# Kernel tuning notes

Hardware: AMD Instinct MI355X
Metric: run time of the kernel (lower is better)

## Reference

```python
import jax, jax.numpy as jnp
import numpy as np

EPS = 1e-5


def setup_inputs() -> dict:
    key = jax.random.key(0)
    ks = jax.random.split(key, 10)
    B, C, H, W = 4, 256, 64, 64
    x = jax.random.normal(ks[0], (B, C, H, W), dtype=jnp.float32)
    s = 1.0 / np.sqrt(C)
    inp = {
        "x": x,
        "gn_w": jnp.ones((C,), jnp.float32),
        "gn_b": jnp.zeros((C,), jnp.float32),
        "wq": jax.random.normal(ks[1], (C, C), jnp.float32) * s,
        "bq": jnp.zeros((C,), jnp.float32),
        "wk": jax.random.normal(ks[2], (C, C), jnp.float32) * s,
        "bk": jnp.zeros((C,), jnp.float32),
        "wv": jax.random.normal(ks[3], (C, C), jnp.float32) * s,
        "bv": jnp.zeros((C,), jnp.float32),
        "wo": jax.random.normal(ks[4], (C, C), jnp.float32) * s,
        "bo": jnp.zeros((C,), jnp.float32),
    }
    return inp


def _forward(x, gn_w, gn_b, wq, bq, wk, bk, wv, bv, wo, bo):
    B, C, H, W = x.shape
    G = C // 2  # num_groups = channels // 2 -> 2 channels per group
    # GroupNorm
    xg = x.reshape(B, G, C // G, H, W)
    mu = jnp.mean(xg, axis=(2, 3, 4), keepdims=True)
    var = jnp.var(xg, axis=(2, 3, 4), keepdims=True)
    hn = ((xg - mu) * jax.lax.rsqrt(var + EPS)).reshape(B, C, H, W)
    hn = hn * gn_w[None, :, None, None] + gn_b[None, :, None, None]
    # tokens: (B, N, C), N = H*W
    h = hn.transpose(0, 2, 3, 1).reshape(B, H * W, C)
    q = h @ wq.T + bq
    k = h @ wk.T + bk
    v = h @ wv.T + bv
    # full NxN attention, scaled by C^-0.5 (as in original)
    scores = jnp.einsum("bnc,bmc->bnm", q, k) * (C ** -0.5)
    attn = jax.nn.softmax(scores, axis=-1)
    h2 = jnp.einsum("bnm,bmc->bnc", attn, v)  # (B, N, C)
    # faithful replication of the original's layout-scrambling reshape:
    # (B,N,C) -> (B,H,W,C) -> permute (B,C,H,W) -> reshape (B,HW,C)
    h2 = h2.reshape(B, H, W, C).transpose(0, 3, 1, 2).reshape(B, H * W, C)
    out = (h2 @ wo.T + bo).reshape(B, C, H, W)
    return x + out


def reference(x, gn_w, gn_b, wq, bq, wk, bk, wv, bv, wo, bo):
    return _forward(x, gn_w, gn_b, wq, bq, wk, bk, wv, bv, wo, bo)
```

## Files before the change

kernel.cpp:

```cpp
#include <hip/hip_runtime.h>

typedef unsigned short u16;
typedef unsigned int   u32;
typedef __attribute__((ext_vector_type(8)))  short short8;
typedef __attribute__((ext_vector_type(4)))  float f32x4;
typedef __attribute__((ext_vector_type(16))) float f32x16;

#define DI __device__ __forceinline__

DI u16 f2bf(float f){
  u32 u = __builtin_bit_cast(u32, f);
  u += 0x7fffu + ((u >> 16) & 1u);
  return (u16)(u >> 16);
}

DI void gl_lds16(const void* g, void* l){
  __builtin_amdgcn_global_load_lds((const __attribute__((address_space(1))) void*)g,
                                   (__attribute__((address_space(3))) void*)l, 16, 0, 0);
}

DI f32x4 mfma16(short8 a, short8 b, f32x4 c){
  return __builtin_amdgcn_mfma_f32_16x16x32_bf16(a, b, c, 0, 0, 0);
}
DI f32x16 mfma32(short8 a, short8 b, f32x16 c){
  return __builtin_amdgcn_mfma_f32_32x32x16_bf16(a, b, c, 0, 0, 0);
}
DI f32x16 z16(){
  f32x16 v;
  #pragma unroll
  for (int i=0;i<16;i++) v[i]=0.f;
  return v;
}

union U8 { u32 u[4]; short8 s; };

#define OFF_WBF   0u
#define OFF_STATS (512u<<10)
#define OFF_HTOK  (1u<<20)
#define OFF_Q     ((1u<<20) + (8u<<20))
#define OFF_K     ((1u<<20) + (16u<<20))
#define OFF_VT    ((1u<<20) + (24u<<20))
#define OFF_H2T   OFF_Q
#define OFF_PART  ((1u<<20) + (32u<<20))
#define OFF_ML    ((1u<<20) + (96u<<20))

__global__ void k_prepstats(const float* wq, const float* wk, const float* wv, const float* wo,
                            u16* wbf, const float* x, float2* stats){
  const int bid = blockIdx.x;
  if (bid < 256){
    const int wi = bid >> 6;
    const float* src = (wi==0)?wq:(wi==1)?wk:(wi==2)?wv:wo;
    u16* d = wbf + wi*65536;
    int i = ((bid&63)*256 + threadIdx.x)*4;
    float4 v = *(const float4*)(src + i);
    u32 lo = (u32)f2bf(v.x) | ((u32)f2bf(v.y)<<16);
    u32 hi = (u32)f2bf(v.z) | ((u32)f2bf(v.w)<<16);
    *(uint2*)(d + i) = make_uint2(lo, hi);
    return;
  }
  const int bg = bid - 256;
  const float* p = x + (size_t)bg*8192;
  float s = 0.f, ss = 0.f;
  #pragma unroll
  for (int i=0;i<8;i++){
    float4 v = *(const float4*)(p + threadIdx.x*4 + i*1024);
    s  += v.x+v.y+v.z+v.w;
    ss += v.x*v.x + v.y*v.y + v.z*v.z + v.w*v.w;
  }
  #pragma unroll
  for (int off=1; off<64; off<<=1){ s += __shfl_xor(s, off, 64); ss += __shfl_xor(ss, off, 64); }
  __shared__ float as[4], aq[4];
  int w = threadIdx.x>>6;
  if ((threadIdx.x&63)==0){ as[w]=s; aq[w]=ss; }
  __syncthreads();
  if (threadIdx.x==0){
    s = as[0]+as[1]+as[2]+as[3]; ss = aq[0]+aq[1]+aq[2]+aq[3];
    float mu = s * (1.f/8192.f);
    float var = ss * (1.f/8192.f) - mu*mu;
    stats[bg] = make_float2(mu, rsqrtf(var + 1e-5f));
  }
}

__global__ void k_gnapply(const float* x, const float* gw, const float* gb,
                          const float2* stats, u16* htok){
  __shared__ u16 tile[64*256];
  int b = blockIdx.y, n0 = blockIdx.x*64, t = threadIdx.x;
  const float* xb = x + (size_t)b*1048576;
  #pragma unroll
  for (int p=0;p<4;p++){
    int c = p*64 + (t>>2);
    float2 st = stats[b*128 + (c>>1)];
    float scl = st.y * gw[c];
    float off = gb[c] - st.x*scl;
    const float* src = xb + (size_t)c*4096 + n0 + (t&3)*16;
    #pragma unroll
    for (int u2=0;u2<4;u2++){
      float4 v = *(const float4*)(src + u2*4);
      float vv[4] = {v.x,v.y,v.z,v.w};
      #pragma unroll
      for (int j=0;j<4;j++){
        int n = (t&3)*16 + u2*4 + j;
        int addr = n*512 + ((c*2) ^ ((n&7)<<4));
        *(u16*)((char*)tile + addr) = f2bf(vv[j]*scl + off);
      }
    }
  }
  __syncthreads();
  int n = t>>2, seg = t&3;
  char* dst = (char*)(htok + ((size_t)(b*4096 + n0 + n)*256 + seg*64));
  #pragma unroll
  for (int i=0;i<8;i++){
    int boff = n*512 + (((seg*128) + i*16) ^ ((n&7)<<4));
    *(uint4*)(dst + i*16) = *(const uint4*)((const char*)tile + boff);
  }
}

__global__ __launch_bounds__(256,2) void k_qkv(const u16* htok, const u16* wbf,
    const float* bq, const float* bk, const float* bv,
    u16* qo, u16* ko, u16* vt){
  __shared__ u16 lds_a[64*256];
  const int t = threadIdx.x, row0 = blockIdx.x*64;
  const int w = t>>6, l = t&63, lo = l&15, hi = l>>4;
  {
    const char* Ab = (const char*)htok + (size_t)row0*512;
    #pragma unroll
    for (int i=0;i<8;i++){
      int row = w*16 + i*2 + (l>>5);
      gl_lds16(Ab + row*512 + (((l&31)*16) ^ ((row&7)<<4)), lds_a + w*4096 + i*512);
    }
    __syncthreads();
  }
  auto compute = [&](const u16* W, f32x4 acc[4][4]){
    #pragma unroll
    for (int i=0;i<4;i++)
      #pragma unroll
      for (int j=0;j<4;j++) acc[i][j] = (f32x4){0.f,0.f,0.f,0.f};
    const char* Wb = (const char*)W;
    #pragma unroll
    for (int dk=0; dk<4; dk++){
      #pragma unroll
      for (int s=0;s<2;s++){
        short8 af[4], bf[4];
        #pragma unroll
        for (int cf=0;cf<4;cf++){
          int col = w*64 + cf*16 + lo;
          bf[cf] = *(const short8*)(Wb + (size_t)col*512 + dk*128 + s*64 + hi*16);
        }
        #pragma unroll
        for (int rg=0;rg<4;rg++){
          int row = rg*16 + lo;
          af[rg] = *(const short8*)((const char*)lds_a + row*512 + ((dk*128 + s*64 + hi*16) ^ ((row&7)<<4)));
        }
        #pragma unroll
        for (int rg=0;rg<4;rg++)
          #pragma unroll
          for (int cf=0;cf<4;cf++)
            acc[rg][cf] = mfma16(af[rg], bf[cf], acc[rg][cf]);
      }
    }
  };
  f32x4 acc[4][4];
  compute(wbf, acc);
  #pragma unroll
  for (int rg=0;rg<4;rg++)
    #pragma unroll
    for (int cf=0;cf<4;cf++){
      int col = w*64 + cf*16 + lo;
      float bs = bq[col];
      #pragma unroll
      for (int r=0;r<4;r++){
        int grow = row0 + rg*16 + hi*4 + r;
        qo[(size_t)grow*256 + col] = f2bf((acc[rg][cf][r] + bs)*0.09016844f);
      }
    }
  compute(wbf + 65536, acc);
  #pragma unroll
  for (int rg=0;rg<4;rg++)
    #pragma unroll
    for (int cf=0;cf<4;cf++){
      int col = w*64 + cf*16 + lo;
      float bs = bk[col];
      #pragma unroll
      for (int r=0;r<4;r++){
        int grow = row0 + rg*16 + hi*4 + r;
        ko[(size_t)grow*256 + col] = f2bf(acc[rg][cf][r] + bs);
      }
    }
  compute(wbf + 2*65536, acc);
  __syncthreads();
  #pragma unroll
  for (int rg=0;rg<4;rg++)
    #pragma unroll
    for (int cf=0;cf<4;cf++){
      int col = w*64 + cf*16 + lo;
      float bs = bv[col];
      ushort4 pk;
      pk.x = f2bf(acc[rg][cf][0]+bs); pk.y = f2bf(acc[rg][cf][1]+bs);
      pk.z = f2bf(acc[rg][cf][2]+bs); pk.w = f2bf(acc[rg][cf][3]+bs);
      int rl = rg*16 + hi*4;
      int addr = col*128 + ((rl*2) ^ ((col&7)<<4));
      *(ushort4*)((char*)lds_a + addr) = pk;
    }
  __syncthreads();
  {
    int b = row0 >> 12, nb = row0 & 4095;
    #pragma unroll
    for (int p=0;p<8;p++){
      int c = p*32 + (t>>3), i = t&7;
      uint4 vd = *(const uint4*)((const char*)lds_a + c*128 + ((i*16) ^ ((c&7)<<4)));
      *(uint4*)((char*)vt + ((size_t)(b*256 + c)*4096 + nb)*2 + i*16) = vd;
    }
  }
}

__global__ __launch_bounds__(256,2) void k_out(const u16* h2t, const u16* wo,
    const float* bo, const float* x, float* out){
  __shared__ u16 lds_a[64*256];
  const int t = threadIdx.x, row0 = blockIdx.x*64;
  const int w = t>>6, l = t&63, lo = l&15, hi = l>>4;
  {
    const char* Ab = (const char*)h2t + (size_t)row0*512;
    #pragma unroll
    for (int i=0;i<8;i++){
      int row = w*16 + i*2 + (l>>5);
      gl_lds16(Ab + row*512 + (((l&31)*16) ^ ((row&7)<<4)), lds_a + w*4096 + i*512);
    }
    __syncthreads();
  }
  f32x4 acc[4][4];
  #pragma unroll
  for (int i=0;i<4;i++)
    #pragma unroll
    for (int j=0;j<4;j++) acc[i][j] = (f32x4){0.f,0.f,0.f,0.f};
  const char* Wb = (const char*)wo;
  #pragma unroll
  for (int dk=0; dk<4; dk++){
    #pragma unroll
    for (int s=0;s<2;s++){
      short8 af[4], bf[4];
      #pragma unroll
      for (int cf=0;cf<4;cf++){
        int col = w*64 + cf*16 + lo;
        bf[cf] = *(const short8*)(Wb + (size_t)col*512 + dk*128 + s*64 + hi*16);
      }
      #pragma unroll
      for (int rg=0;rg<4;rg++){
        int row = rg*16 + lo;
        af[rg] = *(const short8*)((const char*)lds_a + row*512 + ((dk*128 + s*64 + hi*16) ^ ((row&7)<<4)));
      }
      #pragma unroll
      for (int rg=0;rg<4;rg++)
        #pragma unroll
        for (int cf=0;cf<4;cf++)
          acc[rg][cf] = mfma16(af[rg], bf[cf], acc[rg][cf]);
    }
  }
  #pragma unroll
  for (int rg=0;rg<4;rg++)
    #pragma unroll
    for (int cf=0;cf<4;cf++){
      int col = w*64 + cf*16 + lo;
      float bs = bo[col];
      #pragma unroll
      for (int r=0;r<4;r++){
        size_t flat = (size_t)(row0 + rg*16 + hi*4 + r)*256 + col;
        out[flat] = x[flat] + acc[rg][cf][r] + bs;
      }
    }
}

__global__ __launch_bounds__(512,2) void k_attn(const u16* q, const u16* k,
                                                const u16* vt, u16* part, float2* ml){
  __shared__ char smem[131072];
  const int t = threadIdx.x, w = t>>6, l = t&63;
  const int lq = l&31, h = l>>5;
  const int bid = blockIdx.x;
  const int x = bid&7, idx = bid>>3;
  const int combo = x*2 + (idx&1);
  const int b = combo>>2, ks = combo&3, qt = idx>>1;

  const char* kg = (const char*)k  + ((size_t)b*4096 + (size_t)ks*1024)*512;
  const char* vg = (const char*)vt + (size_t)b*2097152 + (size_t)ks*2048;

  short8 qf[16];
  {
    const char* qrow = (const char*)q + ((size_t)b*4096 + qt*256 + w*32 + lq)*512;
    #pragma unroll
    for (int dk=0;dk<16;dk++) qf[dk] = *(const short8*)(qrow + dk*32 + h*16);
  }

  f32x16 O[8];
  #pragma unroll
  for (int ct=0;ct<8;ct++) O[ct] = z16();
  float m_run = -1e30f, l_run = 0.f;

  auto stage = [&](int ti, int buf){
    #pragma unroll
    for (int sub=0; sub<2; ++sub){
      char* kd = smem + buf*32768 + sub*16384;
      char* vd = smem + 65536 + buf*32768 + sub*16384;
      #pragma unroll
      for (int j=0;j<2;j++){
        int key = w*4 + j*2 + h;
        gl_lds16(kg + (size_t)(ti*64 + sub*32 + key)*512 + (((l&31)*16) ^ ((key&7)<<4)),
                 kd + (w*2+j)*1024);
      }
      #pragma unroll
      for (int j=0;j<2;j++){
        int c = w*32 + j*16 + (l>>2);
        gl_lds16(vg + (size_t)c*8192 + ti*128 + sub*64 + (((l&3)*16) ^ (((l>>3)&3)<<4)),
                 vd + (w*2+j)*1024);
      }
    }
  };

  auto smpv = [&](const f32x16& S, const char* vbuf){
    float pmax = S[0];
    #pragma unroll
    for (int r=1;r<16;r++) pmax = fmaxf(pmax, S[r]);
    pmax = fmaxf(pmax, __shfl_xor(pmax, 32, 64));
    if (__any(pmax > m_run + 8.f)){
      float mn = fmaxf(m_run, pmax);
      float sclq = exp2f(m_run - mn);
      m_run = mn;
      l_run *= sclq;
      #pragma unroll
      for (int r=0;r<16;r++){
        float sr = __shfl(sclq, (r&3)+8*(r>>2)+4*h, 64);
        #pragma unroll
        for (int ct=0;ct<8;ct++) O[ct][r] *= sr;
      }
    }
    float p[16]; float ps = 0.f;
    #pragma unroll
    for (int r=0;r<16;r++){ p[r] = exp2f(S[r] - m_run); ps += p[r]; }
    l_run += ps + __shfl_xor(ps, 32, 64);
    u32 pk[8];
    #pragma unroll
    for (int j=0;j<8;j++){
      u32 u0 = __builtin_bit_cast(u32, p[2*j]);
      u32 u1 = __builtin_bit_cast(u32, p[2*j+1]);
      pk[j] = (u1 & 0xffff0000u) | (u0 >> 16);
    }
    #pragma unroll
    for (int kc=0;kc<2;kc++){
      u32 sA = h ? pk[4*kc]   : pk[4*kc+2];
      u32 sB = h ? pk[4*kc+1] : pk[4*kc+3];
      u32 xA = __shfl_xor(sA, 32, 64);
      u32 xB = __shfl_xor(sB, 32, 64);
      U8 pa;
      pa.u[0] = h ? xA : pk[4*kc];
      pa.u[1] = h ? xB : pk[4*kc+1];
      pa.u[2] = h ? pk[4*kc+2] : xA;
      pa.u[3] = h ? pk[4*kc+3] : xB;
      __builtin_amdgcn_s_setprio(1);
      #pragma unroll
      for (int ct=0;ct<8;ct++){
        short8 vb = *(const short8*)(vbuf + (size_t)(ct*32+lq)*64 + ((kc*32 + h*16) ^ (((lq>>1)&3)<<4)));
        O[ct] = mfma32(pa.s, vb, O[ct]);
      }
      __builtin_amdgcn_s_setprio(0);
    }
  };

  stage(0, 0);
  __syncthreads();

  for (int tile=0; tile<16; ++tile){
    const int cur = tile&1;
    if (tile < 15) stage(tile+1, cur^1);
    const char* kbuf0 = smem + cur*32768;
    const char* kbuf1 = kbuf0 + 16384;
    const char* vbuf0 = smem + 65536 + cur*32768;
    const char* vbuf1 = vbuf0 + 16384;

    f32x16 S0 = z16(), S1 = z16();
    __builtin_amdgcn_s_setprio(1);
    #pragma unroll
    for (int dk=0;dk<16;dk++){
      int dby = (dk*32 + h*16) ^ ((lq&7)<<4);
      short8 k0 = *(const short8*)(kbuf0 + (size_t)lq*512 + dby);
      short8 k1 = *(const short8*)(kbuf1 + (size_t)lq*512 + dby);
      S0 = mfma32(k0, qf[dk], S0);
      S1 = mfma32(k1, qf[dk], S1);
    }
    __builtin_amdgcn_s_setprio(0);

    smpv(S0, vbuf0);
    smpv(S1, vbuf1);
    __syncthreads();
  }

  if (h == 0)
    ml[(size_t)combo*4096 + qt*256 + w*32 + lq] = make_float2(m_run, l_run);
  u16* otile = (u16*)smem;
  char* pbase = (char*)part + ((size_t)combo*4096 + (size_t)qt*256)*512;
  #pragma unroll
  for (int rd=0; rd<2; ++rd){
    __syncthreads();
    if ((w>>2) == rd){
      int wl = w&3;
      #pragma unroll
      for (int ct=0;ct<8;ct++)
        #pragma unroll
        for (int r=0;r<16;r++){
          int row = wl*32 + (r&3) + 8*(r>>2) + 4*h;
          otile[row*256 + ct*32 + lq] = f2bf(O[ct][r]);
        }
    }
    __syncthreads();
    const char* sb2 = (const char*)smem;
    char* gb2 = pbase + (size_t)rd*65536;
    #pragma unroll
    for (int j=0;j<8;j++)
      *(uint4*)(gb2 + t*16 + (size_t)j*8192) = *(const uint4*)(sb2 + t*16 + (size_t)j*8192);
  }
}

__global__ __launch_bounds__(256,2) void k_combine(const u16* part, const float2* ml, u16* h2t){
  __shared__ u16 tile[64*256];
  const int t = threadIdx.x, b = blockIdx.y, n0 = blockIdx.x*64;
  const int n = t>>2, cc = (t&3)*64;
  const int gn = n0 + n;
  float2 st[4]; float ms = -1e30f;
  #pragma unroll
  for (int ksi=0;ksi<4;ksi++){ st[ksi] = ml[(size_t)(b*4+ksi)*4096 + gn]; ms = fmaxf(ms, st[ksi].x); }
  float wn[4]; float denom = 0.f;
  #pragma unroll
  for (int ksi=0;ksi<4;ksi++){ wn[ksi] = exp2f(st[ksi].x - ms); denom += wn[ksi]*st[ksi].y; }
  float inv = 1.f/denom;
  #pragma unroll
  for (int ksi=0;ksi<4;ksi++) wn[ksi] *= inv;
  float acc[64];
  #pragma unroll
  for (int j=0;j<64;j++) acc[j] = 0.f;
  #pragma unroll
  for (int ksi=0;ksi<4;ksi++){
    const u16* src = part + ((size_t)(b*4+ksi)*4096 + gn)*256 + cc;
    float wv = wn[ksi];
    #pragma unroll
    for (int j8=0;j8<8;j8++){
      short8 v = *(const short8*)(src + j8*8);
      #pragma unroll
      for (int e=0;e<8;e++){
        u32 uu = ((u32)(u16)v[e])<<16;
        acc[j8*8+e] += wv * __builtin_bit_cast(float, uu);
      }
    }
  }
  char* tb = (char*)tile;
  #pragma unroll
  for (int j=0;j<32;j++){
    u32 pkv = ((u32)f2bf(acc[2*j+1])<<16) | f2bf(acc[2*j]);
    *(u32*)(tb + n*512 + ((cc*2 + j*4) ^ ((n&7)<<4))) = pkv;
  }
  __syncthreads();
  {
    const char* tbc = (const char*)tile;
    u32 outw[32];
    #pragma unroll
    for (int j=0;j<32;j++){
      u16 v0 = *(const u16*)(tbc + (2*j  )*512 + ((t*2) ^ (((2*j  )&7)<<4)));
      u16 v1 = *(const u16*)(tbc + (2*j+1)*512 + ((t*2) ^ (((2*j+1)&7)<<4)));
      outw[j] = ((u32)v1<<16) | v0;
    }
    char* dst = (char*)h2t + ((size_t)(b*256 + t)*4096 + n0)*2;
    #pragma unroll
    for (int j=0;j<8;j++){
      uint4 vv; vv.x = outw[4*j]; vv.y = outw[4*j+1]; vv.z = outw[4*j+2]; vv.w = outw[4*j+3];
      *(uint4*)(dst + j*16) = vv;
    }
  }
}

extern "C" void kernel_launch(void* const* d_in, const int* in_sizes, int n_in,
                              void* d_out, int out_size, void* d_ws, size_t ws_size,
                              hipStream_t stream) {
  const float* x    = (const float*)d_in[0];
  const float* gn_w = (const float*)d_in[1];
  const float* gn_b = (const float*)d_in[2];
  const float* wq   = (const float*)d_in[3];
  const float* bq   = (const float*)d_in[4];
  const float* wk   = (const float*)d_in[5];
  const float* bk   = (const float*)d_in[6];
  const float* wv   = (const float*)d_in[7];
  const float* bv   = (const float*)d_in[8];
  const float* wo   = (const float*)d_in[9];
  const float* bo   = (const float*)d_in[10];
  float* out = (float*)d_out;
  char* ws = (char*)d_ws;

  u16*    wbf   = (u16*)(ws + OFF_WBF);
  float2* stats = (float2*)(ws + OFF_STATS);
  u16*    htok  = (u16*)(ws + OFF_HTOK);
  u16*    qb    = (u16*)(ws + OFF_Q);
  u16*    kb    = (u16*)(ws + OFF_K);
  u16*    vt    = (u16*)(ws + OFF_VT);
  u16*    h2t   = (u16*)(ws + OFF_H2T);
  u16*    part  = (u16*)(ws + OFF_PART);
  float2* ml    = (float2*)(ws + OFF_ML);

  k_prepstats<<<768,      256, 0, stream>>>(wq, wk, wv, wo, wbf, x, stats);
  k_gnapply  <<<dim3(64,4), 256, 0, stream>>>(x, gn_w, gn_b, stats, htok);
  k_qkv      <<<256,      256, 0, stream>>>(htok, wbf, bq, bk, bv, qb, kb, vt);
  k_attn     <<<256,      512, 0, stream>>>(qb, kb, vt, part, ml);
  k_combine  <<<dim3(64,4), 256, 0, stream>>>(part, ml, h2t);
  k_out      <<<256,      256, 0, stream>>>(h2t, wbf + 3*65536, bo, x, out);
}
```

Measured before the change: 167.8 us.

## Fuse split-K attention combine into output projection, store partials channel-major

The attention kernel now writes its per-split partial outputs transposed (channel-major) through a swizzled LDS tile. A new k_outc kernel computes the softmax merge weights from the per-split max/sum stats, combines the four partials directly into an LDS tile, and runs the output projection GEMM, with bias and residual, from that tile. This removes the separate combine kernel, one launch, and the h2t round trip through global memory. In exchange, every output block recomputes merge weights for all 4096 tokens of its batch and keeps them in LDS as fp16, which costs extra work, more LDS and some precision.

```diff
diff --git a/kernel.cpp b/kernel.cpp
--- a/kernel.cpp
+++ b/kernel.cpp
@@ -40,7 +40,6 @@
 #define OFF_Q     ((1u<<20) + (8u<<20))
 #define OFF_K     ((1u<<20) + (16u<<20))
 #define OFF_VT    ((1u<<20) + (24u<<20))
-#define OFF_H2T   OFF_Q
 #define OFF_PART  ((1u<<20) + (32u<<20))
 #define OFF_ML    ((1u<<20) + (96u<<20))
 
@@ -213,62 +212,6 @@
   }
 }
 
-__global__ __launch_bounds__(256,2) void k_out(const u16* h2t, const u16* wo,
-    const float* bo, const float* x, float* out){
-  __shared__ u16 lds_a[64*256];
-  const int t = threadIdx.x, row0 = blockIdx.x*64;
-  const int w = t>>6, l = t&63, lo = l&15, hi = l>>4;
-  {
-    const char* Ab = (const char*)h2t + (size_t)row0*512;
-    #pragma unroll
-    for (int i=0;i<8;i++){
-      int row = w*16 + i*2 + (l>>5);
-      gl_lds16(Ab + row*512 + (((l&31)*16) ^ ((row&7)<<4)), lds_a + w*4096 + i*512);
-    }
-    __syncthreads();
-  }
-  f32x4 acc[4][4];
-  #pragma unroll
-  for (int i=0;i<4;i++)
-    #pragma unroll
-    for (int j=0;j<4;j++) acc[i][j] = (f32x4){0.f,0.f,0.f,0.f};
-  const char* Wb = (const char*)wo;
-  #pragma unroll
-  for (int dk=0; dk<4; dk++){
-    #pragma unroll
-    for (int s=0;s<2;s++){
-      short8 af[4], bf[4];
-      #pragma unroll
-      for (int cf=0;cf<4;cf++){
-        int col = w*64 + cf*16 + lo;
-        bf[cf] = *(const short8*)(Wb + (size_t)col*512 + dk*128 + s*64 + hi*16);
-      }
-      #pragma unroll
-      for (int rg=0;rg<4;rg++){
-        int row = rg*16 + lo;
-        af[rg] = *(const short8*)((const char*)lds_a + row*512 + ((dk*128 + s*64 + hi*16) ^ ((row&7)<<4)));
-      }
-      #pragma unroll
-      for (int rg=0;rg<4;rg++)
-        #pragma unroll
-        for (int cf=0;cf<4;cf++)
-          acc[rg][cf] = mfma16(af[rg], bf[cf], acc[rg][cf]);
-    }
-  }
-  #pragma unroll
-  for (int rg=0;rg<4;rg++)
-    #pragma unroll
-    for (int cf=0;cf<4;cf++){
-      int col = w*64 + cf*16 + lo;
-      float bs = bo[col];
-      #pragma unroll
-      for (int r=0;r<4;r++){
-        size_t flat = (size_t)(row0 + rg*16 + hi*4 + r)*256 + col;
-        out[flat] = x[flat] + acc[rg][cf][r] + bs;
-      }
-    }
-}
-
 __global__ __launch_bounds__(512,2) void k_attn(const u16* q, const u16* k,
                                                 const u16* vt, u16* part, float2* ml){
   __shared__ char smem[131072];
@@ -393,84 +336,144 @@
 
   if (h == 0)
     ml[(size_t)combo*4096 + qt*256 + w*32 + lq] = make_float2(m_run, l_run);
-  u16* otile = (u16*)smem;
-  char* pbase = (char*)part + ((size_t)combo*4096 + (size_t)qt*256)*512;
-  #pragma unroll
-  for (int rd=0; rd<2; ++rd){
-    __syncthreads();
-    if ((w>>2) == rd){
-      int wl = w&3;
-      #pragma unroll
-      for (int ct=0;ct<8;ct++)
-        #pragma unroll
-        for (int r=0;r<16;r++){
-          int row = wl*32 + (r&3) + 8*(r>>2) + 4*h;
-          otile[row*256 + ct*32 + lq] = f2bf(O[ct][r]);
+  {
+    char* ot = smem;
+    #pragma unroll
+    for (int ct=0;ct<8;ct++){
+      int c = ct*32 + lq;
+      char* base = ot + c*512;
+      #pragma unroll
+      for (int rp=0;rp<8;rp++){
+        int r0 = rp*2;
+        int qrow = w*32 + (r0&3) + 8*(r0>>2) + 4*h;
+        u32 val = ((u32)f2bf(O[ct][r0+1])<<16) | f2bf(O[ct][r0]);
+        *(u32*)(base + ((qrow*2) ^ ((c&7)<<4))) = val;
+      }
+    }
+  }
+  __syncthreads();
+  {
+    const char* ot = smem;
+    int c = t>>1, qh = (t&1)*128;
+    char* dst = (char*)part + (((size_t)(combo*256 + c))*4096 + qt*256 + qh)*2;
+    const char* srcb = ot + c*512;
+    int swz = (c&7)<<4;
+    #pragma unroll
+    for (int j=0;j<16;j++){
+      int qoff2 = (qh + j*8)*2;
+      *(uint4*)(dst + j*16) = *(const uint4*)(srcb + (qoff2 ^ swz));
+    }
+  }
+}
+
+__global__ __launch_bounds__(256,2) void k_outc(const u16* part, const float2* ml,
+    const u16* wo, const float* bo, const float* x, float* out){
+  __shared__ u16 lds_a[64*256];
+  __shared__ u16 lds_wn[4*4096];
+  const int t = threadIdx.x, blk = blockIdx.x;
+  const int b = blk>>6, cg = blk&63, row0 = blk*64;
+  const int w = t>>6, l = t&63, lo = l&15, hi = l>>4;
+
+  #pragma unroll
+  for (int i=0;i<16;i++){
+    int n = t + i*256;
+    float2 s0 = ml[(size_t)(b*4+0)*4096 + n];
+    float2 s1 = ml[(size_t)(b*4+1)*4096 + n];
+    float2 s2 = ml[(size_t)(b*4+2)*4096 + n];
+    float2 s3 = ml[(size_t)(b*4+3)*4096 + n];
+    float ms = fmaxf(fmaxf(s0.x, s1.x), fmaxf(s2.x, s3.x));
+    float w0 = exp2f(s0.x - ms), w1 = exp2f(s1.x - ms);
+    float w2 = exp2f(s2.x - ms), w3 = exp2f(s3.x - ms);
+    float inv = 1.f / (w0*s0.y + w1*s1.y + w2*s2.y + w3*s3.y);
+    lds_wn[0*4096 + n] = __builtin_bit_cast(u16, (_Float16)(w0*inv));
+    lds_wn[1*4096 + n] = __builtin_bit_cast(u16, (_Float16)(w1*inv));
+    lds_wn[2*4096 + n] = __builtin_bit_cast(u16, (_Float16)(w2*inv));
+    lds_wn[3*4096 + n] = __builtin_bit_cast(u16, (_Float16)(w3*inv));
+  }
+  __syncthreads();
+
+  {
+    int rr = t>>2, jseg = (t&3)*64;
+    int c = cg*4 + (rr>>4), n0 = (rr&15)*256;
+    #pragma unroll
+    for (int ch=0; ch<4; ++ch){
+      int nb = n0 + jseg + ch*16;
+      float acc[16];
+      #pragma unroll
+      for (int e=0;e<16;e++) acc[e] = 0.f;
+      #pragma unroll
+      for (int ksi=0; ksi<4; ++ksi){
+        const u16* pr = part + ((size_t)((b*4+ksi)*256 + c))*4096 + nb;
+        short8 a0 = *(const short8*)(pr);
+        short8 a1 = *(const short8*)(pr + 8);
+        const u16* wnr = lds_wn + ksi*4096 + nb;
+        short8 w0 = *(const short8*)(wnr);
+        short8 w1 = *(const short8*)(wnr + 8);
+        #pragma unroll
+        for (int e=0;e<8;e++){
+          float av = __builtin_bit_cast(float, ((u32)(u16)a0[e])<<16);
+          float wv = (float)__builtin_bit_cast(_Float16, (u16)w0[e]);
+          acc[e] += wv * av;
         }
-    }
-    __syncthreads();
-    const char* sb2 = (const char*)smem;
-    char* gb2 = pbase + (size_t)rd*65536;
-    #pragma unroll
-    for (int j=0;j<8;j++)
-      *(uint4*)(gb2 + t*16 + (size_t)j*8192) = *(const uint4*)(sb2 + t*16 + (size_t)j*8192);
-  }
-}
-
-__global__ __launch_bounds__(256,2) void k_combine(const u16* part, const float2* ml, u16* h2t){
-  __shared__ u16 tile[64*256];
-  const int t = threadIdx.x, b = blockIdx.y, n0 = blockIdx.x*64;
-  const int n = t>>2, cc = (t&3)*64;
-  const int gn = n0 + n;
-  float2 st[4]; float ms = -1e30f;
-  #pragma unroll
-  for (int ksi=0;ksi<4;ksi++){ st[ksi] = ml[(size_t)(b*4+ksi)*4096 + gn]; ms = fmaxf(ms, st[ksi].x); }
-  float wn[4]; float denom = 0.f;
-  #pragma unroll
-  for (int ksi=0;ksi<4;ksi++){ wn[ksi] = exp2f(st[ksi].x - ms); denom += wn[ksi]*st[ksi].y; }
-  float inv = 1.f/denom;
-  #pragma unroll
-  for (int ksi=0;ksi<4;ksi++) wn[ksi] *= inv;
-  float acc[64];
-  #pragma unroll
-  for (int j=0;j<64;j++) acc[j] = 0.f;
-  #pragma unroll
-  for (int ksi=0;ksi<4;ksi++){
-    const u16* src = part + ((size_t)(b*4+ksi)*4096 + gn)*256 + cc;
-    float wv = wn[ksi];
-    #pragma unroll
-    for (int j8=0;j8<8;j8++){
-      short8 v = *(const short8*)(src + j8*8);
-      #pragma unroll
-      for (int e=0;e<8;e++){
-        u32 uu = ((u32)(u16)v[e])<<16;
-        acc[j8*8+e] += wv * __builtin_bit_cast(float, uu);
-      }
-    }
-  }
-  char* tb = (char*)tile;
-  #pragma unroll
-  for (int j=0;j<32;j++){
-    u32 pkv = ((u32)f2bf(acc[2*j+1])<<16) | f2bf(acc[2*j]);
-    *(u32*)(tb + n*512 + ((cc*2 + j*4) ^ ((n&7)<<4))) = pkv;
-  }
-  __syncthreads();
-  {
-    const char* tbc = (const char*)tile;
-    u32 outw[32];
-    #pragma unroll
-    for (int j=0;j<32;j++){
-      u16 v0 = *(const u16*)(tbc + (2*j  )*512 + ((t*2) ^ (((2*j  )&7)<<4)));
-      u16 v1 = *(const u16*)(tbc + (2*j+1)*512 + ((t*2) ^ (((2*j+1)&7)<<4)));
-      outw[j] = ((u32)v1<<16) | v0;
-    }
-    char* dst = (char*)h2t + ((size_t)(b*256 + t)*4096 + n0)*2;
-    #pragma unroll
-    for (int j=0;j<8;j++){
-      uint4 vv; vv.x = outw[4*j]; vv.y = outw[4*j+1]; vv.z = outw[4*j+2]; vv.w = outw[4*j+3];
-      *(uint4*)(dst + j*16) = vv;
-    }
-  }
+        #pragma unroll
+        for (int e=0;e<8;e++){
+          float av = __builtin_bit_cast(float, ((u32)(u16)a1[e])<<16);
+          float wv = (float)__builtin_bit_cast(_Float16, (u16)w1[e]);
+          acc[8+e] += wv * av;
+        }
+      }
+      char* base = (char*)lds_a + rr*512;
+      int swz = (rr&7)<<4;
+      #pragma unroll
+      for (int e2=0;e2<8;e2++){
+        int jb = (jseg + ch*16 + e2*2)*2;
+        u32 val = ((u32)f2bf(acc[e2*2+1])<<16) | f2bf(acc[e2*2]);
+        *(u32*)(base + (jb ^ swz)) = val;
+      }
+    }
+  }
+  __syncthreads();
+
+  f32x4 acc[4][4];
+  #pragma unroll
+  for (int i=0;i<4;i++)
+    #pragma unroll
+    for (int j=0;j<4;j++) acc[i][j] = (f32x4){0.f,0.f,0.f,0.f};
+  const char* Wb = (const char*)wo;
+  #pragma unroll
+  for (int dk=0; dk<4; dk++){
+    #pragma unroll
+    for (int s=0;s<2;s++){
+      short8 af[4], bf[4];
+      #pragma unroll
+      for (int cf=0;cf<4;cf++){
+        int col = w*64 + cf*16 + lo;
+        bf[cf] = *(const short8*)(Wb + (size_t)col*512 + dk*128 + s*64 + hi*16);
+      }
+      #pragma unroll
+      for (int rg=0;rg<4;rg++){
+        int row = rg*16 + lo;
+        af[rg] = *(const short8*)((const char*)lds_a + row*512 + ((dk*128 + s*64 + hi*16) ^ ((row&7)<<4)));
+      }
+      #pragma unroll
+      for (int rg=0;rg<4;rg++)
+        #pragma unroll
+        for (int cf=0;cf<4;cf++)
+          acc[rg][cf] = mfma16(af[rg], bf[cf], acc[rg][cf]);
+    }
+  }
+  #pragma unroll
+  for (int rg=0;rg<4;rg++)
+    #pragma unroll
+    for (int cf=0;cf<4;cf++){
+      int col = w*64 + cf*16 + lo;
+      float bs = bo[col];
+      #pragma unroll
+      for (int r=0;r<4;r++){
+        size_t flat = (size_t)(row0 + rg*16 + hi*4 + r)*256 + col;
+        out[flat] = x[flat] + acc[rg][cf][r] + bs;
+      }
+    }
 }
 
 extern "C" void kernel_launch(void* const* d_in, const int* in_sizes, int n_in,
@@ -496,14 +499,12 @@
   u16*    qb    = (u16*)(ws + OFF_Q);
   u16*    kb    = (u16*)(ws + OFF_K);
   u16*    vt    = (u16*)(ws + OFF_VT);
-  u16*    h2t   = (u16*)(ws + OFF_H2T);
   u16*    part  = (u16*)(ws + OFF_PART);
   float2* ml    = (float2*)(ws + OFF_ML);
 
-  k_prepstats<<<768,      256, 0, stream>>>(wq, wk, wv, wo, wbf, x, stats);
+  k_prepstats<<<768,        256, 0, stream>>>(wq, wk, wv, wo, wbf, x, stats);
   k_gnapply  <<<dim3(64,4), 256, 0, stream>>>(x, gn_w, gn_b, stats, htok);
-  k_qkv      <<<256,      256, 0, stream>>>(htok, wbf, bq, bk, bv, qb, kb, vt);
-  k_attn     <<<256,      512, 0, stream>>>(qb, kb, vt, part, ml);
-  k_combine  <<<dim3(64,4), 256, 0, stream>>>(part, ml, h2t);
-  k_out      <<<256,      256, 0, stream>>>(h2t, wbf + 3*65536, bo, x, out);
-}
+  k_qkv      <<<256,        256, 0, stream>>>(htok, wbf, bq, bk, bv, qb, kb, vt);
+  k_attn     <<<256,        512, 0, stream>>>(qb, kb, vt, part, ml);
+  k_outc     <<<256,        256, 0, stream>>>(part, ml, wbf + 3*65536, bo, x, out);
+}
```

New measurement: 178.6 us. 6.4% more time.
